# Optimization experiments

Measured on AMD Instinct MI355X. Metric: run time of the kernel, lower is better.

## Reference

```python
import jax, jax.numpy as jnp
import numpy as np

ALPHA = 0.2          # LeakyReLU negative slope
BIG_NEG = -9e15      # mask value used by the torch module
N, FT, C = 8192, 512, 64


def setup_inputs() -> dict:
    key = jax.random.key(0)
    ks = jax.random.split(key, 7)
    features = jax.random.normal(ks[0], (N, FT), jnp.float32)
    W = jax.random.normal(ks[1], (FT, C), jnp.float32) * (1.0 / np.sqrt(FT))
    a = jax.random.normal(ks[2], (2 * C, 1), jnp.float32) * 0.1
    adj1 = jax.random.randint(ks[3], (N, N), 0, 2, jnp.int32)
    adj2 = jax.random.randint(ks[4], (N, N), 0, 2, jnp.int32)
    labels = jax.random.randint(ks[5], (N,), 0, C, jnp.int32)
    idx_train = jax.random.randint(ks[6], (1024,), 0, N, jnp.int32)
    return dict(features=features, W=W, a=a, adj1=adj1, adj2=adj2,
                labels=labels, idx_train=idx_train)


def _gat_layer(h, adj, W, a):
    # Wh: [N, C]
    Wh = h @ W
    c = W.shape[1]
    # The torch code builds an [N, N, 2C] cat tensor then does @ a.
    # That is exactly e_ij = leaky_relu(Wh_i . a[:C] + Wh_j . a[C:]),
    # so compute the two rank-1 terms and broadcast-add instead.
    src = Wh @ a[:c]          # [N, 1] contribution of row node i
    dst = Wh @ a[c:]          # [N, 1] contribution of col node j
    e = jax.nn.leaky_relu(src + dst.T, ALPHA)          # [N, N]
    attn = jax.nn.softmax(jnp.where(adj > 0, e, BIG_NEG), axis=1)
    # dropout is identity in eval mode
    return jax.nn.elu(attn @ Wh)                        # concat=True -> elu


def reference(features, W, a, adj1, adj2, labels, idx_train):
    h_all = jnp.stack(
        [jax.nn.relu(_gat_layer(features, adj, W, a)) for adj in (adj1, adj2)],
        axis=0,
    ).mean(axis=0)                                      # [N, C]
    logits = h_all[idx_train]                           # [n_train, C]
    logp = jax.nn.log_softmax(logits, axis=-1)
    y = labels[idx_train]
    loss = -jnp.take_along_axis(logp, y[:, None], axis=1).mean()
    return loss
```

## Files before the change

### kernel.cpp

```cpp
#include <hip/hip_runtime.h>
#include <hip/hip_bf16.h>


#define NN 8192
#define FTDIM 512
#define CDIM 64
#define NTRAIN 1024
#define LOG2E 1.44269504088896f

typedef __attribute__((ext_vector_type(8))) short short8;
typedef __attribute__((ext_vector_type(4))) float f32x4;
typedef __attribute__((ext_vector_type(4))) int i32x4;

static __device__ __forceinline__ unsigned short f2bf(float x) {
    return __bfloat16_as_ushort(__float2bfloat16(x));
}
static __device__ __forceinline__ float bf2f(unsigned short u) {
    return __uint_as_float((unsigned)u << 16);
}

__global__ __launch_bounds__(256) void k_madj(
    const int* __restrict__ adj1, const int* __restrict__ adj2,
    const int* __restrict__ idxt, const float* __restrict__ W,
    unsigned short* __restrict__ Wt2, unsigned short* __restrict__ maskB,
    float* __restrict__ out)
{
    const int tid = threadIdx.x;

    if (blockIdx.x < 16) {
        const int idx = blockIdx.x * 256 + tid;
        const int kblk = idx >> 6, c = idx & 63;
        short8 v;
#pragma unroll
        for (int e = 0; e < 8; ++e)
            v[e] = (short)f2bf(W[(kblk * 8 + e) * CDIM + c]);
        *(short8*)(Wt2 + (size_t)idx * 8) = v;
        if (blockIdx.x == 0 && tid == 0) out[0] = 0.f;
    }

    const int lane = tid & 63;
    const int w2   = blockIdx.x * 4 + (tid >> 6);
    const int half = w2 & 1;
    const int row  = w2 >> 1;
    const int l    = row >> 10;
    const int ks   = row & 1023;
    const int i    = idxt[ks];

    const int* __restrict__ arow = (l ? adj2 : adj1) + (size_t)i * NN + half * 4096;
    unsigned short* __restrict__ mrow = maskB + (size_t)row * 512 + half * 256;

#pragma unroll
    for (int u = 0; u < 4; ++u) {
        const int lb = u * 1024 + lane * 16;
        const i32x4 a0 = *(const i32x4*)(arow + lb);
        const i32x4 a1 = *(const i32x4*)(arow + lb + 4);
        const i32x4 a2 = *(const i32x4*)(arow + lb + 8);
        const i32x4 a3 = *(const i32x4*)(arow + lb + 12);
        unsigned m = 0;
#pragma unroll
        for (int e = 0; e < 4; ++e) {
            m |= (a0[e] != 0 ? 1u : 0u) << e;
            m |= (a1[e] != 0 ? 1u : 0u) << (4 + e);
            m |= (a2[e] != 0 ? 1u : 0u) << (8 + e);
            m |= (a3[e] != 0 ? 1u : 0u) << (12 + e);
        }
        mrow[u * 64 + lane] = (unsigned short)m;
    }
}

__global__ __launch_bounds__(64) void k_wh(
    const float* __restrict__ feat, const unsigned short* __restrict__ Wt2,
    const float* __restrict__ av, unsigned short* __restrict__ Vt2,
    float4* __restrict__ sQ, float* __restrict__ dE1, float* __restrict__ dE2)
{
    const int lane = threadIdx.x;
    const int r  = lane & 15;
    const int kg = lane >> 4;
    const int row0 = blockIdx.x * 16;

    const float* __restrict__ fp = feat + (size_t)(row0 + r) * FTDIM + kg * 8;

    f32x4 fa[4], fb[4];
#pragma unroll
    for (int d = 0; d < 4; ++d) {
        fa[d] = *(const f32x4*)(fp + d * 32);
        fb[d] = *(const f32x4*)(fp + d * 32 + 4);
    }

    f32x4 acc0 = {0.f, 0.f, 0.f, 0.f};
    f32x4 acc1 = acc0, acc2 = acc0, acc3 = acc0;

    for (int it = 0; it < 16; ++it) {
        const int slot = it & 3;
        const f32x4 a0 = fa[slot], a1 = fb[slot];
        if (it + 4 < 16) {
            fa[slot] = *(const f32x4*)(fp + (it + 4) * 32);
            fb[slot] = *(const f32x4*)(fp + (it + 4) * 32 + 4);
        }

        short8 af;
#pragma unroll
        for (int e = 0; e < 4; ++e) {
            af[e]     = (short)f2bf(a0[e]);
            af[4 + e] = (short)f2bf(a1[e]);
        }

        const unsigned short* bp = Wt2 + ((size_t)(it * 4 + kg)) * 512 + (r << 3);
        const short8 b0 = *(const short8*)(bp);
        const short8 b1 = *(const short8*)(bp + 128);
        const short8 b2 = *(const short8*)(bp + 256);
        const short8 b3 = *(const short8*)(bp + 384);

        acc0 = __builtin_amdgcn_mfma_f32_16x16x32_bf16(af, b0, acc0, 0, 0, 0);
        acc1 = __builtin_amdgcn_mfma_f32_16x16x32_bf16(af, b1, acc1, 0, 0, 0);
        acc2 = __builtin_amdgcn_mfma_f32_16x16x32_bf16(af, b2, acc2, 0, 0, 0);
        acc3 = __builtin_amdgcn_mfma_f32_16x16x32_bf16(af, b3, acc3, 0, 0, 0);
    }

    const size_t jblk = (size_t)(row0 >> 3) + (kg >> 1);
    const int e0 = (kg & 1) * 4;
#pragma unroll
    for (int nt = 0; nt < 4; ++nt) {
        const f32x4 a = (nt == 0) ? acc0 : (nt == 1) ? acc1 : (nt == 2) ? acc2 : acc3;
        ushort4 v4;
        v4.x = f2bf(a[0]); v4.y = f2bf(a[1]); v4.z = f2bf(a[2]); v4.w = f2bf(a[3]);
        *(ushort4*)(Vt2 + jblk * 512 + (size_t)(nt * 16 + r) * 8 + e0) = v4;
    }

    float a1v[4], a2v[4];
#pragma unroll
    for (int nt = 0; nt < 4; ++nt) {
        a1v[nt] = av[nt * 16 + r];
        a2v[nt] = av[CDIM + nt * 16 + r];
    }
#pragma unroll
    for (int q = 0; q < 4; ++q) {
        float s_ = acc0[q] * a1v[0] + acc1[q] * a1v[1]
                 + acc2[q] * a1v[2] + acc3[q] * a1v[3];
        float d_ = acc0[q] * a2v[0] + acc1[q] * a2v[1]
                 + acc2[q] * a2v[2] + acc3[q] * a2v[3];
#pragma unroll
        for (int off = 8; off; off >>= 1) {
            s_ += __shfl_xor(s_, off);
            d_ += __shfl_xor(d_, off);
        }
        if (r == 0) {
            const int i = row0 + kg * 4 + q;
            const float sp = s_ * LOG2E, dp_ = d_ * LOG2E;
            sQ[i] = make_float4(__builtin_amdgcn_exp2f(sp),
                                __builtin_amdgcn_exp2f(0.2f * sp),
                                __builtin_amdgcn_exp2f(-sp), 0.f);
            dE1[i] = __builtin_amdgcn_exp2f(dp_);
            dE2[i] = __builtin_amdgcn_exp2f(0.2f * dp_);
        }
    }
}

struct TileS {
    f32x4 a0, a1, b0, b1;
    short8 v0, v1, v2, v3;
};

template<int SCL>
__global__ __launch_bounds__(256, 4) void k_mattn(
    const unsigned short* __restrict__ maskB,
    const unsigned short* __restrict__ Vt2, const float4* __restrict__ sQ,
    const float* __restrict__ dE1, const float* __restrict__ dE2,
    const int* __restrict__ idxt,
    unsigned short* __restrict__ numPartB, float* __restrict__ zPart)
{
    constexpr int NT = (NN >> SCL) >> 5;
    const int lane = threadIdx.x & 63;
    const int w = (int)((blockIdx.x * blockDim.x + threadIdx.x) >> 6);
    const int l   = w >> (6 + SCL);
    const int rem = w & ((64 << SCL) - 1);
    const int sc  = rem >> 6;
    const int sb  = rem & 63;

    const int r  = lane & 15;
    const int kg = lane >> 4;

    const int ks = sb * 16 + r;
    const int i = idxt[ks];
    const float4 sq = sQ[i];
    const float E1 = sq.x, E2 = sq.y, th = sq.z;

    const int j0 = sc * (NN >> SCL);
    const float* __restrict__ d1p = dE1 + j0 + kg * 8;
    const float* __restrict__ d2p = dE2 + j0 + kg * 8;
    const unsigned short* __restrict__ vbase =
        Vt2 + (((size_t)j0 >> 3) << 9) + ((size_t)kg << 9) + (r << 3);

    const unsigned long long* __restrict__ mptr =
        (const unsigned long long*)((const char*)maskB
            + (size_t)((l << 10) + ks) * 1024 + (j0 >> 3));
    unsigned long long mw[NT / 2];
#pragma unroll
    for (int ww = 0; ww < NT / 2; ++ww) mw[ww] = mptr[ww];

    unsigned mbits[NT];
#pragma unroll
    for (int t = 0; t < NT; ++t)
        mbits[t] = (unsigned)(mw[t >> 1] >> (((t & 1) * 4 + kg) * 8)) & 0xffu;

    short8 bOnes;
#pragma unroll
    for (int e = 0; e < 8; ++e) bOnes[e] = (short)0x3F80;

    f32x4 acc0 = {0.f, 0.f, 0.f, 0.f};
    f32x4 acc1 = acc0, acc2 = acc0, acc3 = acc0, accz = acc0;

    TileS tA, tB;

#define LOADT(T, JT) do { const int _jr = (JT) * 32;                           \
    T.a0 = *(const f32x4*)(d1p + _jr);                                         \
    T.a1 = *(const f32x4*)(d1p + _jr + 4);                                     \
    T.b0 = *(const f32x4*)(d2p + _jr);                                         \
    T.b1 = *(const f32x4*)(d2p + _jr + 4);                                     \
    const unsigned short* _vp = vbase + ((size_t)(JT) << 11);                  \
    T.v0 = *(const short8*)(_vp);                                              \
    T.v1 = *(const short8*)(_vp + 128);                                        \
    T.v2 = *(const short8*)(_vp + 256);                                        \
    T.v3 = *(const short8*)(_vp + 384);                                        \
} while (0)

#define COMPT(T, JT) do {                                                      \
    const unsigned _mb = mbits[JT];                                            \
    short8 af;                                                                 \
    _Pragma("unroll")                                                          \
    for (int e = 0; e < 8; ++e) {                                              \
        const float e1 = (e < 4) ? T.a0[e & 3] : T.a1[e & 3];                  \
        const float e2 = (e < 4) ? T.b0[e & 3] : T.b1[e & 3];                  \
        const bool pos = e1 > th;                                              \
        float p = (pos ? e1 : e2) * (pos ? E1 : E2);                           \
        p = ((_mb >> e) & 1u) ? p : 0.f;                                       \
        af[e] = (short)f2bf(p);                                                \
    }                                                                          \
    acc0 = __builtin_amdgcn_mfma_f32_16x16x32_bf16(af, T.v0, acc0, 0, 0, 0);   \
    acc1 = __builtin_amdgcn_mfma_f32_16x16x32_bf16(af, T.v1, acc1, 0, 0, 0);   \
    acc2 = __builtin_amdgcn_mfma_f32_16x16x32_bf16(af, T.v2, acc2, 0, 0, 0);   \
    acc3 = __builtin_amdgcn_mfma_f32_16x16x32_bf16(af, T.v3, acc3, 0, 0, 0);   \
    accz = __builtin_amdgcn_mfma_f32_16x16x32_bf16(af, bOnes, accz, 0, 0, 0);  \
} while (0)

    LOADT(tA, 0);
#pragma unroll
    for (int jt = 0; jt < NT - 2; jt += 2) {
        LOADT(tB, jt + 1);
        COMPT(tA, jt);
        LOADT(tA, jt + 2);
        COMPT(tB, jt + 1);
    }
    LOADT(tB, NT - 1);
    COMPT(tA, NT - 2);
    COMPT(tB, NT - 1);
#undef LOADT
#undef COMPT

    constexpr int SC = 1 << SCL;
#pragma unroll
    for (int q = 0; q < 4; ++q) {
        const int kss = sb * 16 + kg * 4 + q;
        const size_t slot = ((size_t)kss * 2 + l) * SC + sc;
        unsigned short* op = numPartB + slot * CDIM + r;
        op[0]  = f2bf(acc0[q]);
        op[16] = f2bf(acc1[q]);
        op[32] = f2bf(acc2[q]);
        op[48] = f2bf(acc3[q]);
        if (r == 0) zPart[slot] = accz[q];
    }
}

__global__ __launch_bounds__(256) void k_loss(
    const unsigned short* __restrict__ numPartB, const float* __restrict__ zPart,
    const int* __restrict__ labels, const int* __restrict__ idxt,
    float* __restrict__ out, const int scLog2)
{
    __shared__ float lsum[4];
    const int tid = threadIdx.x;
    const int lane = tid & 63;
    const int wv = tid >> 6;
    const int k = (int)((blockIdx.x * blockDim.x + tid) >> 6);
    const int SC = 1 << scLog2;

    float logit = 0.f;
#pragma unroll
    for (int l = 0; l < 2; ++l) {
        const size_t base = ((size_t)k * 2 + l) * SC;
        float ns = 0.f;
#pragma unroll 16
        for (int s = 0; s < SC; ++s)
            ns += bf2f(numPartB[(base + s) * CDIM + lane]);
        float zs = (lane < SC) ? zPart[base + lane] : 0.f;
#pragma unroll
        for (int off = 32; off; off >>= 1) zs += __shfl_xor(zs, off);
        logit += fmaxf(ns / zs, 0.f);
    }
    logit *= 0.5f;

    float m = logit;
#pragma unroll
    for (int off = 32; off; off >>= 1) m = fmaxf(m, __shfl_xor(m, off));
    float ex = __expf(logit - m);
    float sum = ex;
#pragma unroll
    for (int off = 32; off; off >>= 1) sum += __shfl_xor(sum, off);
    const float logp = logit - m - __logf(sum);

    const int y = labels[idxt[k]];
    const float t = __shfl(logp, y);
    if (lane == 0) lsum[wv] = -t;
    __syncthreads();
    if (tid == 0)
        atomicAdd(out, (lsum[0] + lsum[1] + lsum[2] + lsum[3]) * (1.f / 1024.f));
}

extern "C" void kernel_launch(void* const* d_in, const int* in_sizes, int n_in,
                              void* d_out, int out_size, void* d_ws, size_t ws_size,
                              hipStream_t stream)
{
    const float* feat   = (const float*)d_in[0];
    const float* W      = (const float*)d_in[1];
    const float* av     = (const float*)d_in[2];
    const int*   adj1   = (const int*)d_in[3];
    const int*   adj2   = (const int*)d_in[4];
    const int*   labels = (const int*)d_in[5];
    const int*   idxt   = (const int*)d_in[6];

    const size_t MASKB = 2ull * NTRAIN * (NN / 8);
    const size_t HEAD  = (1u << 20) + (256u << 10) + MASKB;

    auto needed = [&](int scl) -> size_t {
        const size_t SC = (size_t)1 << scl;
        return HEAD + 2 * SC * NTRAIN * CDIM * sizeof(unsigned short)
                    + 2 * SC * NTRAIN * sizeof(float);
    };
    const int scLog2 = (ws_size >= needed(5)) ? 5 : 4;
    const int SC = 1 << scLog2;

    char* ws = (char*)d_ws;
    unsigned short* Vt2 = (unsigned short*)ws;
    unsigned short* Wt2 = (unsigned short*)(ws + (1u << 20));
    float4* sQ  = (float4*)(ws + (1u << 20) + (64u << 10));
    float*  dE1 = (float*)(ws + (1u << 20) + (192u << 10));
    float*  dE2 = (float*)(ws + (1u << 20) + (224u << 10));
    unsigned short* maskB = (unsigned short*)(ws + (1u << 20) + (256u << 10));
    unsigned short* numPartB = (unsigned short*)(ws + HEAD);
    float*  zPart  = (float*)((char*)numPartB
                              + 2ull * SC * NTRAIN * CDIM * sizeof(unsigned short));

    hipLaunchKernelGGL(k_madj, dim3(1024), dim3(256), 0, stream,
                       adj1, adj2, idxt, W, Wt2, maskB, (float*)d_out);
    hipLaunchKernelGGL(k_wh, dim3(512), dim3(64), 0, stream,
                       feat, Wt2, av, Vt2, sQ, dE1, dE2);
    if (scLog2 == 5)
        hipLaunchKernelGGL((k_mattn<5>), dim3(32 * 32), dim3(256), 0, stream,
                           maskB, Vt2, sQ, dE1, dE2, idxt, numPartB, zPart);
    else
        hipLaunchKernelGGL((k_mattn<4>), dim3(32 * 16), dim3(256), 0, stream,
                           maskB, Vt2, sQ, dE1, dE2, idxt, numPartB, zPart);
    hipLaunchKernelGGL(k_loss, dim3(NTRAIN / 4), dim3(256), 0, stream,
                       numPartB, zPart, labels, idxt, (float*)d_out, scLog2);
}
```

Before: 42.24 us.

## Fuse adjacency-mask packing and Wh projection into one front kernel

Merges the mask-packing kernel and the feature projection kernel into a single launch. Blocks below 1024 pack adjacency rows into bitmasks, and the remaining 128 blocks each convert W to bf16 in shared memory, then run four waves of MFMA projection. This removes one kernel launch and the global Wt2 round trip, letting the projection overlap the memory-bound mask work. The cost is that each projection block redoes the W conversion and uses 64KB of LDS, which limits occupancy for those blocks.

```diff
diff --git a/kernel.cpp b/kernel.cpp
--- a/kernel.cpp
+++ b/kernel.cpp
@@ -19,64 +19,69 @@
     return __uint_as_float((unsigned)u << 16);
 }
 
-__global__ __launch_bounds__(256) void k_madj(
+__global__ __launch_bounds__(256) void k_front(
     const int* __restrict__ adj1, const int* __restrict__ adj2,
     const int* __restrict__ idxt, const float* __restrict__ W,
-    unsigned short* __restrict__ Wt2, unsigned short* __restrict__ maskB,
+    const float* __restrict__ feat, const float* __restrict__ av,
+    unsigned short* __restrict__ maskB, unsigned short* __restrict__ Vt2,
+    float4* __restrict__ sQ, float* __restrict__ dE1, float* __restrict__ dE2,
     float* __restrict__ out)
 {
+    __shared__ unsigned short wlds[32768];
+
     const int tid = threadIdx.x;
-
-    if (blockIdx.x < 16) {
-        const int idx = blockIdx.x * 256 + tid;
+    const int bid = blockIdx.x;
+    const int lane = tid & 63;
+
+    if (bid < 1024) {
+        if (bid == 0 && tid == 0) out[0] = 0.f;
+
+        const int w2   = bid * 4 + (tid >> 6);
+        const int half = w2 & 1;
+        const int row  = w2 >> 1;
+        const int l    = row >> 10;
+        const int ks   = row & 1023;
+        const int i    = idxt[ks];
+
+        const int* __restrict__ arow =
+            (l ? adj2 : adj1) + (size_t)i * NN + half * 4096;
+        unsigned short* __restrict__ mrow =
+            maskB + (size_t)row * 512 + half * 256;
+
+#pragma unroll
+        for (int u = 0; u < 4; ++u) {
+            const int lb = u * 1024 + lane * 16;
+            const i32x4 a0 = *(const i32x4*)(arow + lb);
+            const i32x4 a1 = *(const i32x4*)(arow + lb + 4);
+            const i32x4 a2 = *(const i32x4*)(arow + lb + 8);
+            const i32x4 a3 = *(const i32x4*)(arow + lb + 12);
+            unsigned m = 0;
+#pragma unroll
+            for (int e = 0; e < 4; ++e) {
+                m |= (a0[e] != 0 ? 1u : 0u) << e;
+                m |= (a1[e] != 0 ? 1u : 0u) << (4 + e);
+                m |= (a2[e] != 0 ? 1u : 0u) << (8 + e);
+                m |= (a3[e] != 0 ? 1u : 0u) << (12 + e);
+            }
+            mrow[u * 64 + lane] = (unsigned short)m;
+        }
+        return;
+    }
+
+    for (int idx = tid; idx < 4096; idx += 256) {
         const int kblk = idx >> 6, c = idx & 63;
         short8 v;
 #pragma unroll
         for (int e = 0; e < 8; ++e)
             v[e] = (short)f2bf(W[(kblk * 8 + e) * CDIM + c]);
-        *(short8*)(Wt2 + (size_t)idx * 8) = v;
-        if (blockIdx.x == 0 && tid == 0) out[0] = 0.f;
-    }
-
-    const int lane = tid & 63;
-    const int w2   = blockIdx.x * 4 + (tid >> 6);
-    const int half = w2 & 1;
-    const int row  = w2 >> 1;
-    const int l    = row >> 10;
-    const int ks   = row & 1023;
-    const int i    = idxt[ks];
-
-    const int* __restrict__ arow = (l ? adj2 : adj1) + (size_t)i * NN + half * 4096;
-    unsigned short* __restrict__ mrow = maskB + (size_t)row * 512 + half * 256;
-
-#pragma unroll
-    for (int u = 0; u < 4; ++u) {
-        const int lb = u * 1024 + lane * 16;
-        const i32x4 a0 = *(const i32x4*)(arow + lb);
-        const i32x4 a1 = *(const i32x4*)(arow + lb + 4);
-        const i32x4 a2 = *(const i32x4*)(arow + lb + 8);
-        const i32x4 a3 = *(const i32x4*)(arow + lb + 12);
-        unsigned m = 0;
-#pragma unroll
-        for (int e = 0; e < 4; ++e) {
-            m |= (a0[e] != 0 ? 1u : 0u) << e;
-            m |= (a1[e] != 0 ? 1u : 0u) << (4 + e);
-            m |= (a2[e] != 0 ? 1u : 0u) << (8 + e);
-            m |= (a3[e] != 0 ? 1u : 0u) << (12 + e);
-        }
-        mrow[u * 64 + lane] = (unsigned short)m;
-    }
-}
-
-__global__ __launch_bounds__(64) void k_wh(
-    const float* __restrict__ feat, const unsigned short* __restrict__ Wt2,
-    const float* __restrict__ av, unsigned short* __restrict__ Vt2,
-    float4* __restrict__ sQ, float* __restrict__ dE1, float* __restrict__ dE2)
-{
-    const int lane = threadIdx.x;
+        *(short8*)(wlds + (size_t)idx * 8) = v;
+    }
+    __syncthreads();
+
+    const int wv = tid >> 6;
     const int r  = lane & 15;
     const int kg = lane >> 4;
-    const int row0 = blockIdx.x * 16;
+    const int row0 = ((bid - 1024) * 4 + wv) * 16;
 
     const float* __restrict__ fp = feat + (size_t)(row0 + r) * FTDIM + kg * 8;
 
@@ -105,7 +110,7 @@
             af[4 + e] = (short)f2bf(a1[e]);
         }
 
-        const unsigned short* bp = Wt2 + ((size_t)(it * 4 + kg)) * 512 + (r << 3);
+        const unsigned short* bp = wlds + ((size_t)(it * 4 + kg)) * 512 + (r << 3);
         const short8 b0 = *(const short8*)(bp);
         const short8 b1 = *(const short8*)(bp + 128);
         const short8 b2 = *(const short8*)(bp + 256);
@@ -328,7 +333,7 @@
     const int*   idxt   = (const int*)d_in[6];
 
     const size_t MASKB = 2ull * NTRAIN * (NN / 8);
-    const size_t HEAD  = (1u << 20) + (256u << 10) + MASKB;
+    const size_t HEAD  = (1u << 20) + (192u << 10) + MASKB;
 
     auto needed = [&](int scl) -> size_t {
         const size_t SC = (size_t)1 << scl;
@@ -340,19 +345,17 @@
 
     char* ws = (char*)d_ws;
     unsigned short* Vt2 = (unsigned short*)ws;
-    unsigned short* Wt2 = (unsigned short*)(ws + (1u << 20));
-    float4* sQ  = (float4*)(ws + (1u << 20) + (64u << 10));
-    float*  dE1 = (float*)(ws + (1u << 20) + (192u << 10));
-    float*  dE2 = (float*)(ws + (1u << 20) + (224u << 10));
-    unsigned short* maskB = (unsigned short*)(ws + (1u << 20) + (256u << 10));
+    float4* sQ  = (float4*)(ws + (1u << 20));
+    float*  dE1 = (float*)(ws + (1u << 20) + (128u << 10));
+    float*  dE2 = (float*)(ws + (1u << 20) + (160u << 10));
+    unsigned short* maskB = (unsigned short*)(ws + (1u << 20) + (192u << 10));
     unsigned short* numPartB = (unsigned short*)(ws + HEAD);
     float*  zPart  = (float*)((char*)numPartB
                               + 2ull * SC * NTRAIN * CDIM * sizeof(unsigned short));
 
-    hipLaunchKernelGGL(k_madj, dim3(1024), dim3(256), 0, stream,
-                       adj1, adj2, idxt, W, Wt2, maskB, (float*)d_out);
-    hipLaunchKernelGGL(k_wh, dim3(512), dim3(64), 0, stream,
-                       feat, Wt2, av, Vt2, sQ, dE1, dE2);
+    hipLaunchKernelGGL(k_front, dim3(1152), dim3(256), 0, stream,
+                       adj1, adj2, idxt, W, feat, av,
+                       maskB, Vt2, sQ, dE1, dE2, (float*)d_out);
     if (scLog2 == 5)
         hipLaunchKernelGGL((k_mattn<5>), dim3(32 * 32), dim3(256), 0, stream,
                            maskB, Vt2, sQ, dE1, dE2, idxt, numPartB, zPart);
```

New measurement: 46.96 us. 11.2% more time.
